# Performance work log

Hardware: AMD Instinct MI355X
Metric: run time of the kernel (lower is better)

Reference implementation:

```python
import jax, jax.numpy as jnp
import numpy as np

B, T, D = 2, 4096, 768
H = 12
HD = D // H  # 64
SCALE = 1.0 / np.sqrt(HD)


def setup_inputs() -> dict:
    key = jax.random.key(0)
    k1, k2, k3 = jax.random.split(key, 3)
    x = jax.random.normal(k1, (B, T, D), dtype=jnp.float32)
    W_qkv = jax.random.normal(k2, (D, 3 * D), dtype=jnp.float32) * (1.0 / np.sqrt(D))
    b_qkv = jnp.zeros((3 * D,), dtype=jnp.float32)
    W_out = jax.random.normal(k3, (D, D), dtype=jnp.float32) * (1.0 / np.sqrt(D))
    b_out = jnp.zeros((D,), dtype=jnp.float32)
    return {"x": x, "W_qkv": W_qkv, "b_qkv": b_qkv, "W_out": W_out, "b_out": b_out}


def reference(x, W_qkv, b_qkv, W_out, b_out):
    Bx, Tx, C = x.shape
    qkv = x @ W_qkv + b_qkv                                  # [B,T,3D]
    qkv = qkv.reshape(Bx, Tx, 3, H, HD).transpose(2, 0, 3, 1, 4)  # [3,B,H,T,hd]
    q, k, v = qkv[0], qkv[1], qkv[2]
    scores = jnp.einsum('bhqd,bhkd->bhqk', q, k) * SCALE      # [B,H,T,T]
    causal = jnp.tril(jnp.ones((Tx, Tx), dtype=bool))
    scores = jnp.where(causal[None, None], scores, -jnp.inf)
    attn = jax.nn.softmax(scores, axis=-1)
    out = jnp.einsum('bhqk,bhkd->bhqd', attn, v)              # [B,H,T,hd]
    out = out.transpose(0, 2, 1, 3).reshape(Bx, Tx, C)        # [B,T,D]
    return out @ W_out + b_out
```

## Files before the change

### kernel.cpp

```cpp
#include <hip/hip_runtime.h>
#include <cstdint>
#include <cstddef>

typedef _Float16 f16x8 __attribute__((ext_vector_type(8)));
typedef _Float16 f16x4 __attribute__((ext_vector_type(4)));
typedef float    f32x4 __attribute__((ext_vector_type(4)));

#define AS_GLOBAL __attribute__((address_space(1)))
#define AS_LDS    __attribute__((address_space(3)))

__device__ __forceinline__ void load16_to_lds(const _Float16* g, _Float16* l) {
    __builtin_amdgcn_global_load_lds((const AS_GLOBAL void*)g, (AS_LDS void*)l, 16, 0, 0);
}

#define BB   2
#define TT   4096
#define DD   768
#define NH   12
#define HDIM 64
#define D3   2304
#define SC2  (0.125f * 1.44269504088896f)

__global__ __launch_bounds__(256) void prep(const float* __restrict__ x,
                                            _Float16* __restrict__ Xh,
                                            const float* __restrict__ Wqkv,
                                            _Float16* __restrict__ Wqkvt,
                                            const float* __restrict__ Wout,
                                            _Float16* __restrict__ Wot) {
    const int bid = blockIdx.x, tid = threadIdx.x;
    if (bid < 6144) {
        const int i = bid * 1024 + tid * 4;
        float4 v = *(const float4*)(x + i);
        f16x4 h;
        h[0] = (_Float16)v.x; h[1] = (_Float16)v.y;
        h[2] = (_Float16)v.z; h[3] = (_Float16)v.w;
        *(f16x4*)(Xh + i) = h;
        return;
    }
    __shared__ float tile[32][33];
    const float* in; _Float16* out; int C, bx, by;
    if (bid < 7872) {
        const int t = bid - 6144;
        in = Wqkv; out = Wqkvt; C = 2304;
        bx = (t % 72) * 32; by = (t / 72) * 32;
    } else {
        const int t = bid - 7872;
        in = Wout; out = Wot; C = 768;
        bx = (t % 24) * 32; by = (t / 24) * 32;
    }
    const int R = 768;
    const int tx = tid & 31, ty = tid >> 5;
#pragma unroll
    for (int j = 0; j < 32; j += 8)
        tile[ty + j][tx] = in[(size_t)(by + ty + j) * C + bx + tx];
    __syncthreads();
#pragma unroll
    for (int j = 0; j < 32; j += 8)
        out[(size_t)(bx + ty + j) * R + by + tx] = (_Float16)tile[tx][ty + j];
}

template <typename OutT>
__device__ __forceinline__ void gemm_body(const _Float16* __restrict__ A,
                                          const _Float16* __restrict__ Bt,
                                          const float* __restrict__ bias, bool bias_row,
                                          OutT* __restrict__ C, int N, int K,
                                          int m0, int n0,
                                          _Float16* As, _Float16* Bs) {
    const int tid  = threadIdx.x;
    const int wave = tid >> 6, lane = tid & 63, quad = lane >> 4, l16 = lane & 15;
    const int wm = (wave & 1) * 64, wn = (wave >> 1) * 64;
    const int rowc = lane >> 3, part = lane & 7;

    f32x4 acc[4][4];
#pragma unroll
    for (int i = 0; i < 4; ++i)
#pragma unroll
        for (int n = 0; n < 4; ++n) acc[i][n] = f32x4{0.f, 0.f, 0.f, 0.f};

    for (int k0 = 0; k0 < K; k0 += 64) {
        __syncthreads();
#pragma unroll
        for (int cc = 0; cc < 4; ++cc) {
            const int ch = wave * 4 + cc;
            load16_to_lds(A  + (size_t)(m0 + ch * 8 + rowc) * K + k0 + part * 8,
                          As + ch * 512);
            load16_to_lds(Bt + (size_t)(n0 + ch * 8 + rowc) * K + k0 + part * 8,
                          Bs + ch * 512);
        }
        __syncthreads();
#pragma unroll
        for (int i = 0; i < 4; ++i) {
            f16x8 a0 = *(const f16x8*)(As + (wm + i * 16 + l16) * 64 + quad * 8);
            f16x8 a1 = *(const f16x8*)(As + (wm + i * 16 + l16) * 64 + 32 + quad * 8);
#pragma unroll
            for (int n = 0; n < 4; ++n) {
                f16x8 b0 = *(const f16x8*)(Bs + (wn + n * 16 + l16) * 64 + quad * 8);
                f16x8 b1 = *(const f16x8*)(Bs + (wn + n * 16 + l16) * 64 + 32 + quad * 8);
                acc[i][n] = __builtin_amdgcn_mfma_f32_16x16x32_f16(a0, b0, acc[i][n], 0, 0, 0);
                acc[i][n] = __builtin_amdgcn_mfma_f32_16x16x32_f16(a1, b1, acc[i][n], 0, 0, 0);
            }
        }
    }
#pragma unroll
    for (int i = 0; i < 4; ++i)
#pragma unroll
        for (int n = 0; n < 4; ++n)
#pragma unroll
            for (int r = 0; r < 4; ++r) {
                const int row = m0 + wm + i * 16 + quad * 4 + r;
                const int col = n0 + wn + n * 16 + l16;
                const float bv = bias_row ? bias[row] : bias[col];
                C[(size_t)row * N + col] = (OutT)(acc[i][n][r] + bv);
            }
}

__global__ __launch_bounds__(256) void gemm_qkv(const _Float16* __restrict__ Xh,
                                                const _Float16* __restrict__ Wqkvt,
                                                const float* __restrict__ bqkv,
                                                _Float16* __restrict__ QKh,
                                                _Float16* __restrict__ VtG) {
    __shared__ __align__(16) _Float16 As[128 * 64];
    __shared__ __align__(16) _Float16 Bs[128 * 64];
    const int bid = blockIdx.x;
    if (bid < 768) {
        const int bx = bid % 12, by = bid / 12;
        gemm_body<_Float16>(Xh, Wqkvt, bqkv, false, QKh, 1536, DD,
                            by * 128, bx * 128, As, Bs);
    } else {
        const int t = bid - 768;
        const int bx = t % 64, by = t / 64;
        gemm_body<_Float16>(Wqkvt + (size_t)1536 * DD, Xh, bqkv + 1536, true, VtG,
                            8192, DD, by * 128, bx * 128, As, Bs);
    }
}

__global__ __launch_bounds__(256) void gemm_out(const _Float16* __restrict__ A,
                                                const _Float16* __restrict__ Bt,
                                                const float* __restrict__ bias,
                                                float* __restrict__ C) {
    __shared__ __align__(16) _Float16 As[128 * 64];
    __shared__ __align__(16) _Float16 Bs[128 * 64];
    gemm_body<float>(A, Bt, bias, false, C, DD, DD,
                     (int)blockIdx.y * 128, (int)blockIdx.x * 128, As, Bs);
}

__global__ __launch_bounds__(256) void attn_kernel(const _Float16* __restrict__ qk,
                                                   const _Float16* __restrict__ vt,
                                                   _Float16* __restrict__ ao) {
    __shared__ __align__(16) _Float16 Ks[2][64 * 64];
    __shared__ __align__(16) _Float16 Vs[2][64 * 64];
    __shared__ __align__(16) _Float16 Ps[4][16 * 64];

    const int L    = blockIdx.x;
    const int xcd  = L & 7;
    const int r_   = L >> 3;
    const int gIdx = r_ % 3;
    const int qt   = 63 - r_ / 3;
    const int g    = gIdx * 8 + xcd;
    const int b = g / NH, h = g % NH;

    const int tid = threadIdx.x;
    const int wave = tid >> 6, lane = tid & 63, quad = lane >> 4, l16 = lane & 15;

    f16x8 ones;
#pragma unroll
    for (int j = 0; j < 8; ++j) ones[j] = (_Float16)1.0f;

    int vK[2], vV[2];
#pragma unroll
    for (int p = 0; p < 2; ++p) {
        const int j  = wave * 16 + p * 8 + (lane >> 3);
        const int sig = (j & 15) * 4 + (j >> 4);
        const int cdk = (lane & 7) ^ (j & 7);
        vK[p] = (b * TT + sig) * 1536 + DD + h * HDIM + cdk * 8;
        vV[p] = (h * HDIM + j) * 8192 + b * TT + cdk * 8;
    }
    auto stageK = [&](int buf, int k0) {
        const int kK = k0 * 1536;
#pragma unroll
        for (int p = 0; p < 2; ++p)
            load16_to_lds(qk + (vK[p] + kK), Ks[buf] + (wave * 16 + p * 8) * 64);
    };
    auto stageV = [&](int buf, int k0) {
#pragma unroll
        for (int p = 0; p < 2; ++p)
            load16_to_lds(vt + (vV[p] + k0), Vs[buf] + (wave * 16 + p * 8) * 64);
    };

    _Float16* const PsW = &Ps[wave][0];
    _Float16* pw[4];
#pragma unroll
    for (int r = 0; r < 4; ++r) {
        const int row = quad * 4 + r;
        pw[r] = PsW + row * 64 + (((l16 >> 1) ^ (row & 7)) * 8) + (l16 & 1) * 4;
    }
    const _Float16* pr[2];
#pragma unroll
    for (int kh = 0; kh < 2; ++kh)
        pr[kh] = PsW + l16 * 64 + (((kh * 4 + quad) ^ (l16 & 7)) * 8);

    const int q0 = qt * 64;
    const int nkt = qt + 1;
    const int qrow = q0 + wave * 16 + quad * 4;
    f16x8 aq[2];
    {
        const int qoff = (b * TT + q0 + wave * 16 + l16) * 1536 + h * HDIM + quad * 8;
        const _Float16 sc = (_Float16)SC2;
        aq[0] = *(const f16x8*)(qk + qoff) * sc;
        aq[1] = *(const f16x8*)(qk + qoff + 32) * sc;
    }
    f32x4 o[4], lac;
#pragma unroll
    for (int n = 0; n < 4; ++n) o[n] = f32x4{0.f, 0.f, 0.f, 0.f};
    lac = f32x4{0.f, 0.f, 0.f, 0.f};

    auto pv = [&](int vbuf) {
#pragma unroll
        for (int kh = 0; kh < 2; ++kh) {
            f16x8 ap = *(const f16x8*)pr[kh];
            lac = __builtin_amdgcn_mfma_f32_16x16x32_f16(ap, ones, lac, 0, 0, 0);
#pragma unroll
            for (int n = 0; n < 4; ++n) {
                const int posv = (kh * 4 + quad) ^ (l16 & 7);
                f16x8 bv = *(const f16x8*)(Vs[vbuf] + (n * 16 + l16) * 64 + posv * 8);
                o[n] = __builtin_amdgcn_mfma_f32_16x16x32_f16(ap, bv, o[n], 0, 0, 0);
            }
        }
    };

    stageK(0, 0);
    int cur = 0;
    for (int kt = 0; kt < nkt; ++kt) {
        __syncthreads();
        if (kt + 1 < nkt) stageK(cur ^ 1, (kt + 1) * 64);
        stageV(cur, kt * 64);

        __builtin_amdgcn_s_setprio(1);
        f32x4 s[4];
#pragma unroll
        for (int n = 0; n < 4; ++n) s[n] = f32x4{0.f, 0.f, 0.f, 0.f};
#pragma unroll
        for (int kh = 0; kh < 2; ++kh)
#pragma unroll
            for (int n = 0; n < 4; ++n) {
                const int pos = (kh * 4 + quad) ^ (l16 & 7);
                f16x8 bk = *(const f16x8*)(Ks[cur] + (n * 16 + l16) * 64 + pos * 8);
                s[n] = __builtin_amdgcn_mfma_f32_16x16x32_f16(aq[kh], bk, s[n], 0, 0, 0);
            }

        if (kt > 0) pv(cur ^ 1);
        __builtin_amdgcn_s_setprio(0);

        if (kt == nkt - 1) {
#pragma unroll
            for (int n = 0; n < 4; ++n) {
                const int kg = kt * 64 + l16 * 4 + n;
#pragma unroll
                for (int r = 0; r < 4; ++r)
                    if (kg > qrow + r) s[n][r] = -1e30f;
            }
        }

#pragma unroll
        for (int r = 0; r < 4; ++r) {
            f16x4 pk;
#pragma unroll
            for (int n = 0; n < 4; ++n)
                pk[n] = (_Float16)__builtin_amdgcn_exp2f(s[n][r]);
            *(f16x4*)pw[r] = pk;
        }
        cur ^= 1;
    }

    __syncthreads();
    pv(cur ^ 1);

#pragma unroll
    for (int r = 0; r < 4; ++r) {
        const float inv = 1.0f / lac[r];
        const int ooff = (b * TT + qrow + r) * DD + h * HDIM + l16;
#pragma unroll
        for (int n = 0; n < 4; ++n)
            ao[ooff + n * 16] = (_Float16)(o[n][r] * inv);
    }
}

extern "C" void kernel_launch(void* const* d_in, const int* in_sizes, int n_in,
                              void* d_out, int out_size, void* d_ws, size_t ws_size,
                              hipStream_t stream) {
    const float* x     = (const float*)d_in[0];
    const float* Wqkv  = (const float*)d_in[1];
    const float* bqkv  = (const float*)d_in[2];
    const float* Wout  = (const float*)d_in[3];
    const float* bout  = (const float*)d_in[4];
    float* out = (float*)d_out;

    char* ws = (char*)d_ws;
    _Float16* Xh    = (_Float16*)ws;  ws += (size_t)BB * TT * DD * 2;
    _Float16* Wqkvt = (_Float16*)ws;  ws += (size_t)D3 * DD * 2;
    _Float16* Wot   = (_Float16*)ws;  ws += (size_t)DD * DD * 2;
    _Float16* QKh   = (_Float16*)ws;  ws += (size_t)BB * TT * 1536 * 2;
    _Float16* VtG   = (_Float16*)ws;  ws += (size_t)DD * BB * TT * 2;
    _Float16* AOh   = (_Float16*)ws;  ws += (size_t)BB * TT * DD * 2;

    prep<<<8448, 256, 0, stream>>>(x, Xh, Wqkv, Wqkvt, Wout, Wot);

    gemm_qkv<<<1152, 256, 0, stream>>>(Xh, Wqkvt, bqkv, QKh, VtG);

    attn_kernel<<<1536, 256, 0, stream>>>(QKh, VtG, AOh);

    gemm_out<<<dim3(DD / 128, (BB * TT) / 128), 256, 0, stream>>>(AOh, Wot, bout, out);
}
```

Baseline: 246.6 us.

## Enlarge attention query tile to 128 rows and rebalance causal block schedule

Each attention workgroup now handles 128 query rows (32 per wave) instead of 64, so every staged K/V tile feeds twice as many MFMAs and total K/V staging traffic is halved. The grid shrinks to 768 blocks. The block-to-query-tile mapping is replaced by a three-round schedule that pairs long and short causal tiles so per-CU work evens out. The cost is doubled accumulator registers and P-buffer LDS per wave, which may lower occupancy, plus masking on the last two key tiles.

```diff
diff --git a/kernel.cpp b/kernel.cpp
--- a/kernel.cpp
+++ b/kernel.cpp
@@ -149,14 +149,18 @@
                                                    _Float16* __restrict__ ao) {
     __shared__ __align__(16) _Float16 Ks[2][64 * 64];
     __shared__ __align__(16) _Float16 Vs[2][64 * 64];
-    __shared__ __align__(16) _Float16 Ps[4][16 * 64];
-
-    const int L    = blockIdx.x;
-    const int xcd  = L & 7;
-    const int r_   = L >> 3;
-    const int gIdx = r_ % 3;
-    const int qt   = 63 - r_ / 3;
-    const int g    = gIdx * 8 + xcd;
+    __shared__ __align__(16) _Float16 Ps[4][32 * 64];
+
+    const int L   = blockIdx.x;
+    const int xcd = L & 7;
+    const int r_  = L >> 3;
+    const int rnd = r_ >> 5;
+    const int c   = r_ & 31;
+    int qt;
+    if (rnd == 0)      qt = 31 - c;
+    else if (rnd == 1) qt = (c < 16) ? 15 - c : 47 - c;
+    else               qt = (c < 16) ? 2 * c : 2 * c - 31;
+    const int g = rnd * 8 + xcd;
     const int b = g / NH, h = g % NH;
 
     const int tid = threadIdx.x;
@@ -188,42 +192,53 @@
     };
 
     _Float16* const PsW = &Ps[wave][0];
-    _Float16* pw[4];
-#pragma unroll
-    for (int r = 0; r < 4; ++r) {
-        const int row = quad * 4 + r;
-        pw[r] = PsW + row * 64 + (((l16 >> 1) ^ (row & 7)) * 8) + (l16 & 1) * 4;
-    }
-    const _Float16* pr[2];
-#pragma unroll
-    for (int kh = 0; kh < 2; ++kh)
-        pr[kh] = PsW + l16 * 64 + (((kh * 4 + quad) ^ (l16 & 7)) * 8);
-
-    const int q0 = qt * 64;
-    const int nkt = qt + 1;
-    const int qrow = q0 + wave * 16 + quad * 4;
-    f16x8 aq[2];
-    {
-        const int qoff = (b * TT + q0 + wave * 16 + l16) * 1536 + h * HDIM + quad * 8;
+    _Float16* pw[2][4];
+#pragma unroll
+    for (int mq = 0; mq < 2; ++mq)
+#pragma unroll
+        for (int r = 0; r < 4; ++r) {
+            const int row = mq * 16 + quad * 4 + r;
+            pw[mq][r] = PsW + row * 64 + (((l16 >> 1) ^ (row & 7)) * 8) + (l16 & 1) * 4;
+        }
+    const _Float16* pr[2][2];
+#pragma unroll
+    for (int mq = 0; mq < 2; ++mq)
+#pragma unroll
+        for (int kh = 0; kh < 2; ++kh)
+            pr[mq][kh] = PsW + (mq * 16 + l16) * 64 + (((kh * 4 + quad) ^ (l16 & 7)) * 8);
+
+    const int q0 = qt * 128;
+    const int nkt = 2 * qt + 2;
+    const int qrow0 = q0 + wave * 32;
+    f16x8 aq[2][2];
+#pragma unroll
+    for (int mq = 0; mq < 2; ++mq) {
+        const int qoff = (b * TT + qrow0 + mq * 16 + l16) * 1536 + h * HDIM + quad * 8;
         const _Float16 sc = (_Float16)SC2;
-        aq[0] = *(const f16x8*)(qk + qoff) * sc;
-        aq[1] = *(const f16x8*)(qk + qoff + 32) * sc;
-    }
-    f32x4 o[4], lac;
-#pragma unroll
-    for (int n = 0; n < 4; ++n) o[n] = f32x4{0.f, 0.f, 0.f, 0.f};
-    lac = f32x4{0.f, 0.f, 0.f, 0.f};
+        aq[mq][0] = *(const f16x8*)(qk + qoff) * sc;
+        aq[mq][1] = *(const f16x8*)(qk + qoff + 32) * sc;
+    }
+    f32x4 o[2][4], lac[2];
+#pragma unroll
+    for (int mq = 0; mq < 2; ++mq) {
+#pragma unroll
+        for (int n = 0; n < 4; ++n) o[mq][n] = f32x4{0.f, 0.f, 0.f, 0.f};
+        lac[mq] = f32x4{0.f, 0.f, 0.f, 0.f};
+    }
 
     auto pv = [&](int vbuf) {
 #pragma unroll
         for (int kh = 0; kh < 2; ++kh) {
-            f16x8 ap = *(const f16x8*)pr[kh];
-            lac = __builtin_amdgcn_mfma_f32_16x16x32_f16(ap, ones, lac, 0, 0, 0);
+            f16x8 ap0 = *(const f16x8*)pr[0][kh];
+            f16x8 ap1 = *(const f16x8*)pr[1][kh];
+            lac[0] = __builtin_amdgcn_mfma_f32_16x16x32_f16(ap0, ones, lac[0], 0, 0, 0);
+            lac[1] = __builtin_amdgcn_mfma_f32_16x16x32_f16(ap1, ones, lac[1], 0, 0, 0);
 #pragma unroll
             for (int n = 0; n < 4; ++n) {
                 const int posv = (kh * 4 + quad) ^ (l16 & 7);
                 f16x8 bv = *(const f16x8*)(Vs[vbuf] + (n * 16 + l16) * 64 + posv * 8);
-                o[n] = __builtin_amdgcn_mfma_f32_16x16x32_f16(ap, bv, o[n], 0, 0, 0);
+                o[0][n] = __builtin_amdgcn_mfma_f32_16x16x32_f16(ap0, bv, o[0][n], 0, 0, 0);
+                o[1][n] = __builtin_amdgcn_mfma_f32_16x16x32_f16(ap1, bv, o[1][n], 0, 0, 0);
             }
         }
     };
@@ -236,39 +251,48 @@
         stageV(cur, kt * 64);
 
         __builtin_amdgcn_s_setprio(1);
-        f32x4 s[4];
-#pragma unroll
-        for (int n = 0; n < 4; ++n) s[n] = f32x4{0.f, 0.f, 0.f, 0.f};
+        f32x4 s[2][4];
+#pragma unroll
+        for (int mq = 0; mq < 2; ++mq)
+#pragma unroll
+            for (int n = 0; n < 4; ++n) s[mq][n] = f32x4{0.f, 0.f, 0.f, 0.f};
 #pragma unroll
         for (int kh = 0; kh < 2; ++kh)
 #pragma unroll
             for (int n = 0; n < 4; ++n) {
                 const int pos = (kh * 4 + quad) ^ (l16 & 7);
                 f16x8 bk = *(const f16x8*)(Ks[cur] + (n * 16 + l16) * 64 + pos * 8);
-                s[n] = __builtin_amdgcn_mfma_f32_16x16x32_f16(aq[kh], bk, s[n], 0, 0, 0);
+                s[0][n] = __builtin_amdgcn_mfma_f32_16x16x32_f16(aq[0][kh], bk, s[0][n], 0, 0, 0);
+                s[1][n] = __builtin_amdgcn_mfma_f32_16x16x32_f16(aq[1][kh], bk, s[1][n], 0, 0, 0);
             }
 
         if (kt > 0) pv(cur ^ 1);
         __builtin_amdgcn_s_setprio(0);
 
-        if (kt == nkt - 1) {
-#pragma unroll
-            for (int n = 0; n < 4; ++n) {
-                const int kg = kt * 64 + l16 * 4 + n;
-#pragma unroll
-                for (int r = 0; r < 4; ++r)
-                    if (kg > qrow + r) s[n][r] = -1e30f;
-            }
-        }
-
-#pragma unroll
-        for (int r = 0; r < 4; ++r) {
-            f16x4 pk;
-#pragma unroll
-            for (int n = 0; n < 4; ++n)
-                pk[n] = (_Float16)__builtin_amdgcn_exp2f(s[n][r]);
-            *(f16x4*)pw[r] = pk;
-        }
+        if (kt >= nkt - 2) {
+#pragma unroll
+            for (int mq = 0; mq < 2; ++mq) {
+                const int qr = qrow0 + mq * 16 + quad * 4;
+#pragma unroll
+                for (int n = 0; n < 4; ++n) {
+                    const int kg = kt * 64 + l16 * 4 + n;
+#pragma unroll
+                    for (int r = 0; r < 4; ++r)
+                        if (kg > qr + r) s[mq][n][r] = -1e30f;
+                }
+            }
+        }
+
+#pragma unroll
+        for (int mq = 0; mq < 2; ++mq)
+#pragma unroll
+            for (int r = 0; r < 4; ++r) {
+                f16x4 pk;
+#pragma unroll
+                for (int n = 0; n < 4; ++n)
+                    pk[n] = (_Float16)__builtin_amdgcn_exp2f(s[mq][n][r]);
+                *(f16x4*)pw[mq][r] = pk;
+            }
         cur ^= 1;
     }
 
@@ -276,13 +300,15 @@
     pv(cur ^ 1);
 
 #pragma unroll
-    for (int r = 0; r < 4; ++r) {
-        const float inv = 1.0f / lac[r];
-        const int ooff = (b * TT + qrow + r) * DD + h * HDIM + l16;
-#pragma unroll
-        for (int n = 0; n < 4; ++n)
-            ao[ooff + n * 16] = (_Float16)(o[n][r] * inv);
-    }
+    for (int mq = 0; mq < 2; ++mq)
+#pragma unroll
+        for (int r = 0; r < 4; ++r) {
+            const float inv = 1.0f / lac[mq][r];
+            const int ooff = (b * TT + qrow0 + mq * 16 + quad * 4 + r) * DD + h * HDIM + l16;
+#pragma unroll
+            for (int n = 0; n < 4; ++n)
+                ao[ooff + n * 16] = (_Float16)(o[mq][n][r] * inv);
+        }
 }
 
 extern "C" void kernel_launch(void* const* d_in, const int* in_sizes, int n_in,
@@ -307,7 +333,7 @@
 
     gemm_qkv<<<1152, 256, 0, stream>>>(Xh, Wqkvt, bqkv, QKh, VtG);
 
-    attn_kernel<<<1536, 256, 0, stream>>>(QKh, VtG, AOh);
+    attn_kernel<<<768, 256, 0, stream>>>(QKh, VtG, AOh);
 
     gemm_out<<<dim3(DD / 128, (BB * TT) / 128), 256, 0, stream>>>(AOh, Wot, bout, out);
 }
```

Measured after the change: 273.7 us. 1.11x slower.
